# Kernel optimization log

Measured on AMD Instinct MI355X. Metric: run time of the kernel, lower is better.

## Reference

```python
import jax, jax.numpy as jnp
import numpy as np

# BiDAF-style co-attention with memory_len=2. Dropout is inference-mode identity.

def setup_inputs() -> dict:
    key = jax.random.key(0)
    k1, k2, k3, k4, k5 = jax.random.split(key, 5)
    d = 1024
    inp = jax.random.normal(k1, (8, 4096, d), dtype=jnp.float32)
    mem = jax.random.normal(k2, (8, 2, d), dtype=jnp.float32)
    w_input = jax.random.normal(k3, (d,), dtype=jnp.float32) * (1.0 / np.sqrt(d))
    w_memory = jax.random.normal(k4, (d,), dtype=jnp.float32) * (1.0 / np.sqrt(d))
    dot_scale = jax.random.uniform(k5, (d,), dtype=jnp.float32, minval=0.0, maxval=1.0 / np.sqrt(d))
    return {"input": inp, "memory": mem, "w_input": w_input, "w_memory": w_memory, "dot_scale": dot_scale}


def reference(input, memory, w_input, w_memory, dot_scale):
    # input: [b, L, d]; memory: [b, M=2, d]
    input_dot = jnp.einsum('bld,d->bl', input, w_input)[..., None]        # [b, L, 1]
    memory_dot = jnp.einsum('bmd,d->bm', memory, w_memory)[:, None, :]    # [b, 1, M]
    cross_dot = jnp.einsum('bld,bmd->blm', input * dot_scale, memory)     # [b, L, M]
    att = input_dot + memory_dot + cross_dot                              # [b, L, M]
    weight_one = jax.nn.softmax(att, axis=-1)                             # [b, L, M]
    output_one = jnp.einsum('blm,bmd->bld', weight_one, memory)           # [b, L, d]
    weight_two = jax.nn.softmax(jnp.max(att, axis=-1), axis=-1)           # [b, L]
    output_two = jnp.einsum('bl,bld->bd', weight_two, input)[:, None, :]  # [b, 1, d]
    return jnp.concatenate([input, output_one, input * output_one, output_two * output_one], axis=-1)
```

## Files before the change

### kernel.cpp

```cpp
#include <hip/hip_runtime.h>
#include <stdint.h>


#define BB 8
#define LL 4096
#define DD 1024
#define NBLK 2048
#define BPB 256
#define RPB 16
#define RPW 4

typedef float f32x4 __attribute__((ext_vector_type(4)));

static __device__ __forceinline__ f32x4 nt_load4(const float* p) {
    return __builtin_nontemporal_load((const f32x4*)p);
}
static __device__ __forceinline__ void nt_store4(float* p, f32x4 v) {
    __builtin_nontemporal_store(v, (f32x4*)p);
}
static __device__ __forceinline__ float hsum4(f32x4 v) {
    return (v.x + v.y) + (v.z + v.w);
}

__global__ __launch_bounds__(256) void kA(const float* __restrict__ input,
                                          const float* __restrict__ memory,
                                          const float* __restrict__ w_in,
                                          const float* __restrict__ w_mem,
                                          const float* __restrict__ ds,
                                          float* __restrict__ w0buf,
                                          float* __restrict__ pmax,
                                          float* __restrict__ pz,
                                          float* __restrict__ pacc,
                                          float* __restrict__ out) {
    int blk = blockIdx.x;
    int b = blk >> 8, chunk = blk & 255;
    int t = threadIdx.x;
    int wave = t >> 6, lane = t & 63;

    f32x4 rc0[4], rc1[4], rm0[4], rm1[4], acc[4];
    float md0 = 0.f, md1 = 0.f;
    {
        const float* m0p = memory + (size_t)b * 2 * DD;
        const float* m1p = m0p + DD;
#pragma unroll
        for (int k = 0; k < 4; ++k) {
            int i = 4 * (lane + 64 * k);
            f32x4 m0 = *(const f32x4*)(m0p + i);
            f32x4 m1 = *(const f32x4*)(m1p + i);
            f32x4 wi = *(const f32x4*)(w_in + i);
            f32x4 dv = *(const f32x4*)(ds + i);
            f32x4 wm = *(const f32x4*)(w_mem + i);
            rm0[k] = m0; rm1[k] = m1;
            rc0[k] = wi + dv * m0;
            rc1[k] = wi + dv * m1;
            md0 += hsum4(m0 * wm);
            md1 += hsum4(m1 * wm);
            acc[k] = (f32x4)(0.f);
        }
        for (int off = 32; off; off >>= 1) {
            md0 += __shfl_xor(md0, off);
            md1 += __shfl_xor(md1, off);
        }
    }

    float lmax = -1e30f, zsum = 0.f;
    int l0 = chunk * RPB + wave * RPW;
    const float* inb = input + (size_t)b * LL * DD;
    for (int r = 0; r < RPW; ++r) {
        int l = l0 + r;
        const float* row = inb + (size_t)l * DD;
        f32x4 x[4];
#pragma unroll
        for (int k = 0; k < 4; ++k) x[k] = nt_load4(row + 4 * (lane + 64 * k));

        f32x4 s0 = x[0] * rc0[0], s1 = x[0] * rc1[0];
#pragma unroll
        for (int k = 1; k < 4; ++k) { s0 += x[k] * rc0[k]; s1 += x[k] * rc1[k]; }
        float a0 = hsum4(s0), a1 = hsum4(s1);
        for (int off = 32; off; off >>= 1) {
            a0 += __shfl_xor(a0, off);
            a1 += __shfl_xor(a1, off);
        }
        a0 += md0; a1 += md1;

        float w0 = 1.f / (1.f + __expf(a1 - a0));
        float w1 = 1.f - w0;
        if (lane == 0) w0buf[(size_t)b * LL + l] = w0;
        float ml = fmaxf(a0, a1);

        float e;
        if (ml > lmax) {
            float s = __expf(lmax - ml);
            zsum *= s;
#pragma unroll
            for (int k = 0; k < 4; ++k) acc[k] *= s;
            lmax = ml;
            e = 1.f;
        } else {
            e = __expf(ml - lmax);
        }
        zsum += e;

        float* orow = out + (size_t)(b * LL + l) * (4 * DD);
        f32x4 o1v[4];
#pragma unroll
        for (int k = 0; k < 4; ++k) o1v[k] = w0 * rm0[k] + w1 * rm1[k];
#pragma unroll
        for (int k = 0; k < 4; ++k)
            nt_store4(orow + 4 * (lane + 64 * k), x[k]);
#pragma unroll
        for (int k = 0; k < 4; ++k)
            nt_store4(orow + DD + 4 * (lane + 64 * k), o1v[k]);
#pragma unroll
        for (int k = 0; k < 4; ++k)
            nt_store4(orow + 2 * DD + 4 * (lane + 64 * k), x[k] * o1v[k]);
#pragma unroll
        for (int k = 0; k < 4; ++k) acc[k] += e * x[k];
    }

    __shared__ float swm[4], swz[4];
    __shared__ __align__(16) float swacc[4][DD];
    if (lane == 0) { swm[wave] = lmax; swz[wave] = zsum; }
    __syncthreads();
    float bmax = fmaxf(fmaxf(swm[0], swm[1]), fmaxf(swm[2], swm[3]));
    float f = __expf(lmax - bmax);
#pragma unroll
    for (int k = 0; k < 4; ++k) {
        *(f32x4*)(swacc[wave] + 4 * (lane + 64 * k)) = f * acc[k];
    }
    __syncthreads();
    {
        f32x4 s = *(const f32x4*)(swacc[0] + 4 * t) + *(const f32x4*)(swacc[1] + 4 * t)
                + *(const f32x4*)(swacc[2] + 4 * t) + *(const f32x4*)(swacc[3] + 4 * t);
        *(f32x4*)(pacc + (size_t)blk * DD + 4 * t) = s;
        if (t == 0) {
            float bz = 0.f;
#pragma unroll
            for (int w = 0; w < 4; ++w) bz += swz[w] * __expf(swm[w] - bmax);
            pmax[blk] = bmax;
            pz[blk]   = bz;
        }
    }
}

__global__ __launch_bounds__(256) void kB(const float* __restrict__ pmax,
                                          const float* __restrict__ pz,
                                          const float* __restrict__ pacc,
                                          float* __restrict__ out2) {
    int bid = blockIdx.x;
    int b = bid >> 2, q = bid & 3;
    int t = threadIdx.x;
    int d = q * 256 + t;
    __shared__ float se[BPB];
    const float* pm  = pmax + b * BPB;
    const float* pzb = pz   + b * BPB;
    float m = -1e30f;
    for (int i = 0; i < BPB; ++i) m = fmaxf(m, pm[i]);
    se[t] = __expf(pm[t] - m);
    __syncthreads();
    float Z = 0.f;
    for (int i = 0; i < BPB; ++i) Z = fmaf(pzb[i], se[i], Z);
    float invZ = 1.f / Z;

    const float* P = pacc + (size_t)b * BPB * DD + d;
    float a = 0.f;
    for (int i = 0; i < BPB; ++i) a = fmaf(se[i], P[(size_t)i * DD], a);
    out2[(size_t)b * DD + d] = a * invZ;
}

__global__ __launch_bounds__(256) void kE(const float* __restrict__ memory,
                                          const float* __restrict__ w0buf,
                                          const float* __restrict__ out2,
                                          float* __restrict__ out) {
    int bid = blockIdx.x;
    int b = bid >> 9, chunk = bid & 511;
    int t = threadIdx.x;
    f32x4 m0 = *(const f32x4*)(memory + (size_t)b * 2 * DD + 4 * t);
    f32x4 m1 = *(const f32x4*)(memory + (size_t)b * 2 * DD + DD + 4 * t);
    f32x4 o2 = *(const f32x4*)(out2 + (size_t)b * DD + 4 * t);
    const float* w0b = w0buf + (size_t)b * LL + chunk * 8;
    for (int r = 0; r < 8; ++r) {
        float w0 = w0b[r];
        float w1 = 1.f - w0;
        f32x4 o1 = w0 * m0 + w1 * m1;
        float* orow = out + (size_t)(b * LL + chunk * 8 + r) * (4 * DD) + 3 * DD;
        nt_store4(orow + 4 * t, o2 * o1);
    }
}

extern "C" void kernel_launch(void* const* d_in, const int* in_sizes, int n_in,
                              void* d_out, int out_size, void* d_ws, size_t ws_size,
                              hipStream_t stream) {
    const float* input  = (const float*)d_in[0];
    const float* memory = (const float*)d_in[1];
    const float* w_in   = (const float*)d_in[2];
    const float* w_mem  = (const float*)d_in[3];
    const float* ds     = (const float*)d_in[4];
    float* out = (float*)d_out;

    float* ws    = (float*)d_ws;
    float* w0buf = ws;
    float* pmax  = ws + 32768;
    float* pz    = ws + 34816;
    float* out2  = ws + 36864;
    float* pacc  = ws + 45056;

    kA<<<NBLK, 256, 0, stream>>>(input, memory, w_in, w_mem, ds,
                                 w0buf, pmax, pz, pacc, out);
    kB<<<32,   256, 0, stream>>>(pmax, pz, pacc, out2);
    kE<<<4096, 256, 0, stream>>>(memory, w0buf, out2, out);
}
```

Before: 646.7 us.

## Split input pass into reduction-only kernel and full-row output writer kernel

The first kernel now only computes attention weights and the partial softmax-weighted sums, and uses cached loads instead of nontemporal ones. A new final kernel re-reads the input and writes all four output segments of each row contiguously, replacing the separate strided write of the last segment. The aim is to take the heavy store traffic out of the reduction pass and to write whole output rows in one place. In exchange the input is read twice, and this relies on the second read hitting in L2 or the large last-level cache.

```diff
diff --git a/kernel.cpp b/kernel.cpp
--- a/kernel.cpp
+++ b/kernel.cpp
@@ -5,10 +5,12 @@
 #define BB 8
 #define LL 4096
 #define DD 1024
-#define NBLK 2048
+#define NBLK1 2048
 #define BPB 256
 #define RPB 16
 #define RPW 4
+#define NBLK2 4096
+#define RPB2 8
 
 typedef float f32x4 __attribute__((ext_vector_type(4)));
 
@@ -22,22 +24,21 @@
     return (v.x + v.y) + (v.z + v.w);
 }
 
-__global__ __launch_bounds__(256) void kA(const float* __restrict__ input,
-                                          const float* __restrict__ memory,
-                                          const float* __restrict__ w_in,
-                                          const float* __restrict__ w_mem,
-                                          const float* __restrict__ ds,
-                                          float* __restrict__ w0buf,
-                                          float* __restrict__ pmax,
-                                          float* __restrict__ pz,
-                                          float* __restrict__ pacc,
-                                          float* __restrict__ out) {
+__global__ __launch_bounds__(256) void kA1(const float* __restrict__ input,
+                                           const float* __restrict__ memory,
+                                           const float* __restrict__ w_in,
+                                           const float* __restrict__ w_mem,
+                                           const float* __restrict__ ds,
+                                           float* __restrict__ w0buf,
+                                           float* __restrict__ pmax,
+                                           float* __restrict__ pz,
+                                           float* __restrict__ pacc) {
     int blk = blockIdx.x;
     int b = blk >> 8, chunk = blk & 255;
     int t = threadIdx.x;
     int wave = t >> 6, lane = t & 63;
 
-    f32x4 rc0[4], rc1[4], rm0[4], rm1[4], acc[4];
+    f32x4 rc0[4], rc1[4], acc[4];
     float md0 = 0.f, md1 = 0.f;
     {
         const float* m0p = memory + (size_t)b * 2 * DD;
@@ -50,7 +51,6 @@
             f32x4 wi = *(const f32x4*)(w_in + i);
             f32x4 dv = *(const f32x4*)(ds + i);
             f32x4 wm = *(const f32x4*)(w_mem + i);
-            rm0[k] = m0; rm1[k] = m1;
             rc0[k] = wi + dv * m0;
             rc1[k] = wi + dv * m1;
             md0 += hsum4(m0 * wm);
@@ -71,7 +71,7 @@
         const float* row = inb + (size_t)l * DD;
         f32x4 x[4];
 #pragma unroll
-        for (int k = 0; k < 4; ++k) x[k] = nt_load4(row + 4 * (lane + 64 * k));
+        for (int k = 0; k < 4; ++k) x[k] = *(const f32x4*)(row + 4 * (lane + 64 * k));
 
         f32x4 s0 = x[0] * rc0[0], s1 = x[0] * rc1[0];
 #pragma unroll
@@ -84,7 +84,6 @@
         a0 += md0; a1 += md1;
 
         float w0 = 1.f / (1.f + __expf(a1 - a0));
-        float w1 = 1.f - w0;
         if (lane == 0) w0buf[(size_t)b * LL + l] = w0;
         float ml = fmaxf(a0, a1);
 
@@ -100,20 +99,6 @@
             e = __expf(ml - lmax);
         }
         zsum += e;
-
-        float* orow = out + (size_t)(b * LL + l) * (4 * DD);
-        f32x4 o1v[4];
-#pragma unroll
-        for (int k = 0; k < 4; ++k) o1v[k] = w0 * rm0[k] + w1 * rm1[k];
-#pragma unroll
-        for (int k = 0; k < 4; ++k)
-            nt_store4(orow + 4 * (lane + 64 * k), x[k]);
-#pragma unroll
-        for (int k = 0; k < 4; ++k)
-            nt_store4(orow + DD + 4 * (lane + 64 * k), o1v[k]);
-#pragma unroll
-        for (int k = 0; k < 4; ++k)
-            nt_store4(orow + 2 * DD + 4 * (lane + 64 * k), x[k] * o1v[k]);
 #pragma unroll
         for (int k = 0; k < 4; ++k) acc[k] += e * x[k];
     }
@@ -168,23 +153,30 @@
     out2[(size_t)b * DD + d] = a * invZ;
 }
 
-__global__ __launch_bounds__(256) void kE(const float* __restrict__ memory,
-                                          const float* __restrict__ w0buf,
-                                          const float* __restrict__ out2,
-                                          float* __restrict__ out) {
+__global__ __launch_bounds__(256) void kA2(const float* __restrict__ input,
+                                           const float* __restrict__ memory,
+                                           const float* __restrict__ w0buf,
+                                           const float* __restrict__ out2,
+                                           float* __restrict__ out) {
     int bid = blockIdx.x;
     int b = bid >> 9, chunk = bid & 511;
     int t = threadIdx.x;
     f32x4 m0 = *(const f32x4*)(memory + (size_t)b * 2 * DD + 4 * t);
     f32x4 m1 = *(const f32x4*)(memory + (size_t)b * 2 * DD + DD + 4 * t);
     f32x4 o2 = *(const f32x4*)(out2 + (size_t)b * DD + 4 * t);
-    const float* w0b = w0buf + (size_t)b * LL + chunk * 8;
-    for (int r = 0; r < 8; ++r) {
+    const float* w0b = w0buf + (size_t)b * LL + chunk * RPB2;
+    const float* inb = input + (size_t)(b * LL + chunk * RPB2) * DD;
+#pragma unroll 2
+    for (int r = 0; r < RPB2; ++r) {
         float w0 = w0b[r];
         float w1 = 1.f - w0;
+        f32x4 x = nt_load4(inb + (size_t)r * DD + 4 * t);
         f32x4 o1 = w0 * m0 + w1 * m1;
-        float* orow = out + (size_t)(b * LL + chunk * 8 + r) * (4 * DD) + 3 * DD;
-        nt_store4(orow + 4 * t, o2 * o1);
+        float* orow = out + (size_t)(b * LL + chunk * RPB2 + r) * (4 * DD);
+        nt_store4(orow + 4 * t, x);
+        nt_store4(orow + DD + 4 * t, o1);
+        nt_store4(orow + 2 * DD + 4 * t, x * o1);
+        nt_store4(orow + 3 * DD + 4 * t, o2 * o1);
     }
 }
 
@@ -205,8 +197,8 @@
     float* out2  = ws + 36864;
     float* pacc  = ws + 45056;
 
-    kA<<<NBLK, 256, 0, stream>>>(input, memory, w_in, w_mem, ds,
-                                 w0buf, pmax, pz, pacc, out);
-    kB<<<32,   256, 0, stream>>>(pmax, pz, pacc, out2);
-    kE<<<4096, 256, 0, stream>>>(memory, w0buf, out2, out);
-}
+    kA1<<<NBLK1, 256, 0, stream>>>(input, memory, w_in, w_mem, ds,
+                                   w0buf, pmax, pz, pacc);
+    kB <<<32,    256, 0, stream>>>(pmax, pz, pacc, out2);
+    kA2<<<NBLK2, 256, 0, stream>>>(input, memory, w0buf, out2, out);
+}
```

After: 651.0 us. No clear change (+0.7%).
